# Kernel optimization log

Hardware: AMD Instinct MI355X
Metric: run time of the kernel (lower is better)

The kernel has to match this reference:

```python
import jax, jax.numpy as jnp
import numpy as np
from jax import lax

B, T, D, H, O = 4096, 128, 128, 150, 10

def setup_inputs() -> dict:
    key = jax.random.key(0)
    k1, k2, k3 = jax.random.split(key, 3)
    X = jax.random.normal(k1, (B, T, D), dtype=jnp.float32)
    # BasicRNNCell kernel: acts on concat([x, h]) -> [D+H, H]
    W_cell = jax.random.normal(k2, (D + H, H), dtype=jnp.float32) * (1.0 / np.sqrt(D + H))
    b_cell = jnp.zeros((H,), dtype=jnp.float32)
    W_out = jax.random.normal(k3, (H, O), dtype=jnp.float32) * (1.0 / np.sqrt(H))
    b_out = jnp.zeros((O,), dtype=jnp.float32)
    return {"X": X, "W_cell": W_cell, "b_cell": b_cell, "W_out": W_out, "b_out": b_out}

def reference(X, W_cell, b_cell, W_out, b_out):
    # dynamic_rnn with BasicRNNCell: h_t = tanh([x_t, h_{t-1}] @ W + b)
    batch = X.shape[0]
    hid = W_cell.shape[1]
    xs = jnp.swapaxes(X, 0, 1)  # [T, B, D]
    h0 = jnp.zeros((batch, hid), dtype=X.dtype)

    def step(h, x_t):
        h_new = jnp.tanh(jnp.concatenate([x_t, h], axis=-1) @ W_cell + b_cell)
        return h_new, None

    h_final, _ = lax.scan(step, h0, xs)
    # dense classifier on final state (tf code applies dense to `states`)
    logits = h_final @ W_out + b_out  # [B, O]
    return logits
```

## Files before the change

### kernel.cpp

```cpp
#include <hip/hip_runtime.h>
#include <hip/hip_bf16.h>


typedef __bf16 bf16x8 __attribute__((ext_vector_type(8)));
typedef float  f32x4  __attribute__((ext_vector_type(4)));
typedef float  f32x8  __attribute__((ext_vector_type(8)));
typedef unsigned short u16;

#define B_  4096
#define T_  128
#define D_  128
#define H_  150
#define O_  10

#define KX 4
#define KH 5
#define HPAD 168

__global__ __launch_bounds__(320, 2) void rnn_fused(
    const float* __restrict__ X,
    const float* __restrict__ Wc,
    const float* __restrict__ bc,
    const float* __restrict__ Wo,
    const float* __restrict__ bo,
    float* __restrict__ out)
{
    __shared__ __attribute__((aligned(16))) __bf16 sh_h[2][16][HPAD];

    const int tid  = threadIdx.x;
    const int wid  = tid >> 6;
    const int lane = tid & 63;
    const int q    = lane >> 4;
    const int l16  = lane & 15;
    const int row0 = blockIdx.x * 16;

    {
        __bf16* p = &sh_h[0][0][0];
        for (int i = tid; i < 2 * 16 * HPAD; i += 320) p[i] = (__bf16)0.f;
    }

    bf16x8 wx[2][KX];
    bf16x8 wh[2][KH];
    float  bias[2];
    const int colw = wid * 32 + 2 * l16;
#pragma unroll
    for (int nt = 0; nt < 2; ++nt) {
        const int  j   = colw + nt;
        const bool jv  = (j < H_);
        const int  jcl = jv ? j : 0;
        bias[nt] = jv ? bc[jcl] : 0.f;
#pragma unroll
        for (int kt = 0; kt < KX; ++kt) {
            bf16x8 f;
#pragma unroll
            for (int i = 0; i < 8; ++i) {
                const int k = kt * 32 + q * 8 + i;
                float v = Wc[k * H_ + jcl];
                v = fminf(fmaxf(v, -64.f), 64.f);
                f[i] = jv ? (__bf16)v : (__bf16)0.f;
            }
            wx[nt][kt] = f;
        }
#pragma unroll
        for (int kt = 0; kt < KH; ++kt) {
            bf16x8 f;
#pragma unroll
            for (int i = 0; i < 8; ++i) {
                const int  kh  = kt * 32 + q * 8 + i;
                const bool kv  = jv && (kh < H_);
                const int  khc = (kh < H_) ? kh : 0;
                float v = Wc[(D_ + khc) * H_ + jcl];
                v = fminf(fmaxf(v, -64.f), 64.f);
                f[i] = kv ? (__bf16)v : (__bf16)0.f;
            }
            wh[nt][kt] = f;
        }
    }

    __syncthreads();

    const float* xrow = X + (size_t)(row0 + l16) * (T_ * D_) + q * 8;

    f32x8 xb0[KX], xb1[KX];
#pragma unroll
    for (int kt = 0; kt < KX; ++kt) xb0[kt] = *(const f32x8*)(xrow + 0 * D_ + kt * 32);
#pragma unroll
    for (int kt = 0; kt < KX; ++kt) xb1[kt] = *(const f32x8*)(xrow + 1 * D_ + kt * 32);

    auto step = [&](int t, f32x8 (&xb)[KX]) {
        const __bf16 (*hb)[HPAD] = sh_h[t & 1];
        bf16x8 ah[KH];
#pragma unroll
        for (int kt = 0; kt < KH; ++kt)
            ah[kt] = *(const bf16x8*)(&hb[l16][kt * 32 + q * 8]);

        bf16x8 a[KX];
#pragma unroll
        for (int kt = 0; kt < KX; ++kt) {
#pragma unroll
            for (int i = 0; i < 8; ++i)
                a[kt][i] = (__bf16)xb[kt][i];
        }

        {
            int tt = t + 2; tt = (tt > T_ - 1) ? (T_ - 1) : tt;
#pragma unroll
            for (int kt = 0; kt < KX; ++kt)
                xb[kt] = *(const f32x8*)(xrow + (size_t)tt * D_ + kt * 32);
        }

        f32x4 ax0 = {bias[0], bias[0], bias[0], bias[0]};
        f32x4 ax1 = {bias[1], bias[1], bias[1], bias[1]};
        f32x4 ah0 = {0.f, 0.f, 0.f, 0.f};
        f32x4 ah1 = {0.f, 0.f, 0.f, 0.f};
#pragma unroll
        for (int kt = 0; kt < KX; ++kt) {
            ax0 = __builtin_amdgcn_mfma_f32_16x16x32_bf16(a[kt], wx[0][kt], ax0, 0, 0, 0);
            ax1 = __builtin_amdgcn_mfma_f32_16x16x32_bf16(a[kt], wx[1][kt], ax1, 0, 0, 0);
        }
#pragma unroll
        for (int kt = 0; kt < KH; ++kt) {
            ah0 = __builtin_amdgcn_mfma_f32_16x16x32_bf16(ah[kt], wh[0][kt], ah0, 0, 0, 0);
            ah1 = __builtin_amdgcn_mfma_f32_16x16x32_bf16(ah[kt], wh[1][kt], ah1, 0, 0, 0);
        }

        __bf16 (*ho)[HPAD] = sh_h[(t + 1) & 1];
#pragma unroll
        for (int r = 0; r < 4; ++r) {
            const float z0 = ax0[r] + ah0[r];
            const float z1 = ax1[r] + ah1[r];
            const float e0 = __builtin_amdgcn_exp2f(z0 * 2.8853900817779268f);
            const float e1 = __builtin_amdgcn_exp2f(z1 * 2.8853900817779268f);
            const float h0 = 1.f - 2.f * __builtin_amdgcn_rcpf(e0 + 1.f);
            const float h1 = 1.f - 2.f * __builtin_amdgcn_rcpf(e1 + 1.f);
            const unsigned p = (unsigned)__builtin_bit_cast(u16, (__bf16)h0)
                             | ((unsigned)__builtin_bit_cast(u16, (__bf16)h1) << 16);
            *(unsigned*)(&ho[q * 4 + r][colw]) = p;
        }

        asm volatile("s_waitcnt lgkmcnt(0)\n\ts_barrier" ::: "memory");
    };

    for (int t = 0; t < T_; t += 2) {
        step(t,     xb0);
        step(t + 1, xb1);
    }

    __syncthreads();

    if (tid < 16 * O_) {
        const int row = tid / O_;
        const int o   = tid - row * O_;
        float accv = bo[o];
        const __bf16* hf = &sh_h[0][row][0];
        for (int k = 0; k < H_; ++k)
            accv += (float)hf[k] * Wo[k * O_ + o];
        out[(size_t)(row0 + row) * O_ + o] = accv;
    }
}

extern "C" void kernel_launch(void* const* d_in, const int* in_sizes, int n_in,
                              void* d_out, int out_size, void* d_ws, size_t ws_size,
                              hipStream_t stream) {
    (void)in_sizes; (void)n_in; (void)out_size; (void)d_ws; (void)ws_size;
    const float* X  = (const float*)d_in[0];
    const float* Wc = (const float*)d_in[1];
    const float* bc = (const float*)d_in[2];
    const float* Wo = (const float*)d_in[3];
    const float* bo = (const float*)d_in[4];
    rnn_fused<<<dim3(B_ / 16), dim3(320), 0, stream>>>(X, Wc, bc, Wo, bo, (float*)d_out);
}
```

Baseline: 455.9 us.

## Redistribute hidden-column tiles across four waves instead of five

Cuts the block from 5 to 4 waves. Two waves now compute three 16-column output tiles and two waves compute two, still covering all 160 padded hidden columns. With one wave per SIMD, no SIMD has to run two waves' worth of MFMAs in each serial recurrence step, and the per-step barrier has fewer participants. In exchange, the three-tile waves carry more weight registers and a longer dependent MFMA chain per step.

```diff
diff --git a/kernel.cpp b/kernel.cpp
--- a/kernel.cpp
+++ b/kernel.cpp
@@ -17,7 +17,7 @@
 #define KH 5
 #define HPAD 168
 
-__global__ __launch_bounds__(320, 2) void rnn_fused(
+__global__ __launch_bounds__(256, 1) void rnn_fused(
     const float* __restrict__ X,
     const float* __restrict__ Wc,
     const float* __restrict__ bc,
@@ -34,20 +34,26 @@
     const int l16  = lane & 15;
     const int row0 = blockIdx.x * 16;
 
+    const int nt_cnt = (wid < 2) ? 3 : 2;
+    const int tbase  = (wid < 2) ? wid * 3 : 6 + (wid - 2) * 2;
+    const int cbase  = tbase * 16;
+
     {
         __bf16* p = &sh_h[0][0][0];
-        for (int i = tid; i < 2 * 16 * HPAD; i += 320) p[i] = (__bf16)0.f;
+        for (int i = tid; i < 2 * 16 * HPAD; i += 256) p[i] = (__bf16)0.f;
     }
 
-    bf16x8 wx[2][KX];
-    bf16x8 wh[2][KH];
-    float  bias[2];
-    const int colw = wid * 32 + 2 * l16;
+    bf16x8 wx[3][KX];
+    bf16x8 wh[3][KH];
+    float  bias[3];
+    int    jc[3];
 #pragma unroll
-    for (int nt = 0; nt < 2; ++nt) {
-        const int  j   = colw + nt;
+    for (int nt = 0; nt < 3; ++nt) {
+        if (nt >= nt_cnt) break;
+        const int  j   = (nt < 2) ? (cbase + 2 * l16 + nt) : (cbase + 32 + l16);
         const bool jv  = (j < H_);
         const int  jcl = jv ? j : 0;
+        jc[nt]   = j;
         bias[nt] = jv ? bc[jcl] : 0.f;
 #pragma unroll
         for (int kt = 0; kt < KX; ++kt) {
@@ -109,33 +115,47 @@
                 xb[kt] = *(const f32x8*)(xrow + (size_t)tt * D_ + kt * 32);
         }
 
-        f32x4 ax0 = {bias[0], bias[0], bias[0], bias[0]};
-        f32x4 ax1 = {bias[1], bias[1], bias[1], bias[1]};
-        f32x4 ah0 = {0.f, 0.f, 0.f, 0.f};
-        f32x4 ah1 = {0.f, 0.f, 0.f, 0.f};
+        f32x4 ax[3], ahh[3];
+#pragma unroll
+        for (int nt = 0; nt < 3; ++nt) {
+            if (nt >= nt_cnt) break;
+            ax[nt]  = (f32x4){bias[nt], bias[nt], bias[nt], bias[nt]};
+            ahh[nt] = (f32x4){0.f, 0.f, 0.f, 0.f};
+        }
 #pragma unroll
         for (int kt = 0; kt < KX; ++kt) {
-            ax0 = __builtin_amdgcn_mfma_f32_16x16x32_bf16(a[kt], wx[0][kt], ax0, 0, 0, 0);
-            ax1 = __builtin_amdgcn_mfma_f32_16x16x32_bf16(a[kt], wx[1][kt], ax1, 0, 0, 0);
+            ax[0] = __builtin_amdgcn_mfma_f32_16x16x32_bf16(a[kt], wx[0][kt], ax[0], 0, 0, 0);
+            ax[1] = __builtin_amdgcn_mfma_f32_16x16x32_bf16(a[kt], wx[1][kt], ax[1], 0, 0, 0);
+            if (nt_cnt == 3)
+                ax[2] = __builtin_amdgcn_mfma_f32_16x16x32_bf16(a[kt], wx[2][kt], ax[2], 0, 0, 0);
         }
 #pragma unroll
         for (int kt = 0; kt < KH; ++kt) {
-            ah0 = __builtin_amdgcn_mfma_f32_16x16x32_bf16(ah[kt], wh[0][kt], ah0, 0, 0, 0);
-            ah1 = __builtin_amdgcn_mfma_f32_16x16x32_bf16(ah[kt], wh[1][kt], ah1, 0, 0, 0);
+            ahh[0] = __builtin_amdgcn_mfma_f32_16x16x32_bf16(ah[kt], wh[0][kt], ahh[0], 0, 0, 0);
+            ahh[1] = __builtin_amdgcn_mfma_f32_16x16x32_bf16(ah[kt], wh[1][kt], ahh[1], 0, 0, 0);
+            if (nt_cnt == 3)
+                ahh[2] = __builtin_amdgcn_mfma_f32_16x16x32_bf16(ah[kt], wh[2][kt], ahh[2], 0, 0, 0);
         }
 
         __bf16 (*ho)[HPAD] = sh_h[(t + 1) & 1];
 #pragma unroll
         for (int r = 0; r < 4; ++r) {
-            const float z0 = ax0[r] + ah0[r];
-            const float z1 = ax1[r] + ah1[r];
+            const int rr = q * 4 + r;
+            const float z0 = ax[0][r] + ahh[0][r];
+            const float z1 = ax[1][r] + ahh[1][r];
             const float e0 = __builtin_amdgcn_exp2f(z0 * 2.8853900817779268f);
             const float e1 = __builtin_amdgcn_exp2f(z1 * 2.8853900817779268f);
             const float h0 = 1.f - 2.f * __builtin_amdgcn_rcpf(e0 + 1.f);
             const float h1 = 1.f - 2.f * __builtin_amdgcn_rcpf(e1 + 1.f);
             const unsigned p = (unsigned)__builtin_bit_cast(u16, (__bf16)h0)
                              | ((unsigned)__builtin_bit_cast(u16, (__bf16)h1) << 16);
-            *(unsigned*)(&ho[q * 4 + r][colw]) = p;
+            *(unsigned*)(&ho[rr][cbase + 2 * l16]) = p;
+            if (nt_cnt == 3) {
+                const float z2 = ax[2][r] + ahh[2][r];
+                const float e2 = __builtin_amdgcn_exp2f(z2 * 2.8853900817779268f);
+                const float h2 = 1.f - 2.f * __builtin_amdgcn_rcpf(e2 + 1.f);
+                ho[rr][cbase + 32 + l16] = (__bf16)h2;
+            }
         }
 
         asm volatile("s_waitcnt lgkmcnt(0)\n\ts_barrier" ::: "memory");
@@ -168,5 +188,5 @@
     const float* bc = (const float*)d_in[2];
     const float* Wo = (const float*)d_in[3];
     const float* bo = (const float*)d_in[4];
-    rnn_fused<<<dim3(B_ / 16), dim3(320), 0, stream>>>(X, Wc, bc, Wo, bo, (float*)d_out);
+    rnn_fused<<<dim3(B_ / 16), dim3(256), 0, stream>>>(X, Wc, bc, Wo, bo, (float*)d_out);
 }
```

Measured after the change: 434.8 us. 1.05x faster.
